# Kernel tuning notes

Hardware: AMD Instinct MI355X
Metric: run time of the kernel (lower is better)

## Reference

```python
import jax, jax.numpy as jnp
import numpy as np

B = 4096
LT = 30        # title_length
LE = 10        # max_entity_num
D = 300        # word/entity embedding dim
WORD_NUM = 100000
VERT_NUM = 18
H1, D1 = 20, 20   # Attention(20, 20) -> 400
H2, D2 = 5, 40    # Attention(5, 40)  -> 200
FUSE = H1 * D1 + H2 * D2   # 600
OUT = 400


def setup_inputs():
    key = jax.random.key(0)
    ks = jax.random.split(key, 24)
    s = 0.02
    inp = {
        'title_ids': jax.random.randint(ks[0], (B, LT), 0, WORD_NUM),
        'vert_ids': jax.random.randint(ks[1], (B,), 0, VERT_NUM + 1),
        'entity_ids': jax.random.randint(ks[2], (B, LE), 0, WORD_NUM),
        'word_table': jax.random.normal(ks[3], (WORD_NUM + 1, D), jnp.float32) * s,
        'vert_table': jax.random.normal(ks[4], (VERT_NUM + 1, 200), jnp.float32) * s,
        'entity_table': jax.random.normal(ks[5], (WORD_NUM, D), jnp.float32) * s,
        'WQ': jax.random.normal(ks[6], (D, H1 * D1), jnp.float32) * s,
        'WK': jax.random.normal(ks[7], (D, H1 * D1), jnp.float32) * s,
        'WV': jax.random.normal(ks[8], (D, H1 * D1), jnp.float32) * s,
        'WQ2': jax.random.normal(ks[9], (D, H2 * D2), jnp.float32) * s,
        'WK2': jax.random.normal(ks[10], (D, H2 * D2), jnp.float32) * s,
        'WV2': jax.random.normal(ks[11], (D, H2 * D2), jnp.float32) * s,
        'fc1_W': jax.random.normal(ks[12], (FUSE, OUT), jnp.float32) * s,
        'fc1_b': jnp.zeros((OUT,), jnp.float32),
        'fc2_W': jax.random.normal(ks[13], (FUSE, OUT), jnp.float32) * s,
        'fc2_b': jnp.zeros((OUT,), jnp.float32),
        'apt_W1': jax.random.normal(ks[14], (OUT, 200), jnp.float32) * s,
        'apt_b1': jnp.zeros((200,), jnp.float32),
        'apt_w2': jax.random.normal(ks[15], (200,), jnp.float32) * s,
        'ape_W1': jax.random.normal(ks[16], (OUT, 200), jnp.float32) * s,
        'ape_b1': jnp.zeros((200,), jnp.float32),
        'ape_w2': jax.random.normal(ks[17], (200,), jnp.float32) * s,
        'fc3_W': jax.random.normal(ks[18], (OUT + OUT + 200, OUT), jnp.float32) * s,
        'fc3_b': jnp.zeros((OUT,), jnp.float32),
    }
    return inp


def _mha(q_in, k_in, v_in, WQ, WK, WV, h, d):
    # q_in: [B,Lq,D]; k_in/v_in: [B,Lk,D] -> out [B,Lq,h*d]
    b, lq, _ = q_in.shape
    lk = k_in.shape[1]
    Q = (q_in @ WQ).reshape(b, lq, h, d)
    K = (k_in @ WK).reshape(b, lk, h, d)
    V = (v_in @ WV).reshape(b, lk, h, d)
    scores = jnp.einsum('bqhd,bkhd->bhqk', Q, K) / jnp.sqrt(jnp.asarray(d, Q.dtype))
    attn = jax.nn.softmax(scores, axis=-1)
    out = jnp.einsum('bhqk,bkhd->bqhd', attn, V)
    return out.reshape(b, lq, h * d)


def _att_pool(x, W1, b1, w2):
    # x: [B,L,F] -> [B,F]
    a = jax.nn.softmax(jnp.tanh(x @ W1 + b1) @ w2, axis=1)  # [B,L]
    return jnp.einsum('bl,blf->bf', a, x)


def reference(title_ids, vert_ids, entity_ids, word_table, vert_table, entity_table,
              WQ, WK, WV, WQ2, WK2, WV2, fc1_W, fc1_b, fc2_W, fc2_b,
              apt_W1, apt_b1, apt_w2, ape_W1, ape_b1, ape_w2, fc3_W, fc3_b):
    # Dropout is identity at inference.
    vert_vec = vert_table[vert_ids]              # [B,200]
    title_emb = word_table[title_ids]            # [B,LT,D]
    entity_emb = entity_table[entity_ids]        # [B,LE,D]

    # Cross (co-)attention, shared Attention2(5,40) weights
    title_co = _mha(title_emb, entity_emb, entity_emb, WQ2, WK2, WV2, H2, D2)   # [B,LT,200]
    entity_co = _mha(entity_emb, title_emb, title_emb, WQ2, WK2, WV2, H2, D2)   # [B,LE,200]

    # Self attention, shared Attention(20,20) weights
    title_vecs = _mha(title_emb, title_emb, title_emb, WQ, WK, WV, H1, D1)      # [B,LT,400]
    title_vecs = jnp.concatenate([title_vecs, title_co], axis=-1) @ fc1_W + fc1_b  # [B,LT,400]
    title_vec = _att_pool(title_vecs, apt_W1, apt_b1, apt_w2)                   # [B,400]

    entity_vecs = _mha(entity_emb, entity_emb, entity_emb, WQ, WK, WV, H1, D1)  # [B,LE,400]
    entity_vecs = jnp.concatenate([entity_vecs, entity_co], axis=-1) @ fc2_W + fc2_b
    entity_vec = _att_pool(entity_vecs, ape_W1, ape_b1, ape_w2)                 # [B,400]

    news_vec = jnp.concatenate([title_vec, entity_vec, vert_vec], axis=-1)      # [B,1000]
    return news_vec @ fc3_W + fc3_b                                             # [B,400]
```

## Files before the change

kernel.cpp:

```cpp
#include <hip/hip_runtime.h>
#include <hip/hip_bf16.h>

typedef unsigned short u16b;
typedef __attribute__((ext_vector_type(8))) short bf16x8;
typedef __attribute__((ext_vector_type(4))) float f32x4;

__device__ __forceinline__ float b2f(u16b u) { return __uint_as_float(((unsigned)u) << 16); }
__device__ __forceinline__ u16b f2b(float f) {
    unsigned u = __float_as_uint(f);
    unsigned r = u + 0x7fffu + ((u >> 16) & 1u);
    return (u16b)(r >> 16);
}
__device__ __forceinline__ int pk2(float a, float b) {
    return (int)f2b(a) | ((int)f2b(b) << 16);
}

__device__ __forceinline__ void async16(const u16b* g, u16b* l) {
    __builtin_amdgcn_global_load_lds(
        (const __attribute__((address_space(1))) unsigned int*)g,
        (__attribute__((address_space(3))) unsigned int*)l,
        16, 0, 0);
}

#define BATCH 4096
#define NPROJ 1920

__global__ void pack_wcatT(const float* __restrict__ WQ, const float* __restrict__ WK,
                           const float* __restrict__ WV, const float* __restrict__ WQ2,
                           const float* __restrict__ WK2, const float* __restrict__ WV2,
                           u16b* __restrict__ Wt) {
    int idx = blockIdx.x * 256 + threadIdx.x;
    if (idx >= 1920 * 320) return;
    int n = idx / 320, k = idx % 320;
    float v = 0.0f;
    if (k < 300 && n < 1800) {
        if      (n < 400)  v = WQ [k * 400 + n];
        else if (n < 800)  v = WK [k * 400 + (n - 400)];
        else if (n < 1200) v = WV [k * 400 + (n - 800)];
        else if (n < 1400) v = WQ2[k * 200 + (n - 1200)];
        else if (n < 1600) v = WK2[k * 200 + (n - 1400)];
        else               v = WV2[k * 200 + (n - 1600)];
    }
    Wt[idx] = f2b(v);
}

__global__ void pack_wt(const float* __restrict__ W, u16b* __restrict__ Wt,
                        int K, int N, int Kp, int Npad) {
    int idx = blockIdx.x * 256 + threadIdx.x;
    if (idx >= Npad * Kp) return;
    int n = idx / Kp, k = idx % Kp;
    Wt[idx] = f2b((k < K && n < N) ? W[k * N + n] : 0.0f);
}

__global__ void gather_bf16(const int* __restrict__ ids, const float* __restrict__ table,
                            u16b* __restrict__ Abuf, int nrows) {
    int idx = blockIdx.x * 256 + threadIdx.x;
    if (idx >= nrows * 40) return;
    int row = idx / 40, c = idx % 40;
    int k = c * 8;
    const float* src = table + (long long)ids[row] * 300;
    int4 v;
    if (k + 8 <= 300) {
        float4 f0 = *(const float4*)(src + k);
        float4 f1 = *(const float4*)(src + k + 4);
        v.x = pk2(f0.x, f0.y); v.y = pk2(f0.z, f0.w);
        v.z = pk2(f1.x, f1.y); v.w = pk2(f1.z, f1.w);
    } else if (k < 300) {
        float f[8];
        #pragma unroll
        for (int i = 0; i < 8; i++) f[i] = (k + i < 300) ? src[k + i] : 0.0f;
        v.x = pk2(f[0], f[1]); v.y = pk2(f[2], f[3]);
        v.z = pk2(f[4], f[5]); v.w = pk2(f[6], f[7]);
    } else {
        v.x = v.y = v.z = v.w = 0;
    }
    *(int4*)(Abuf + (long long)row * 320 + k) = v;
}

template<int HAS_BIAS, int DO_TANH>
__global__ __launch_bounds__(256) void gemm_mfma2(
        const u16b* __restrict__ A, long long lda,
        const u16b* __restrict__ Wt, int ldwt,
        const float* __restrict__ Bias,
        u16b* __restrict__ Out, long long ldo,
        int kiters, int N) {
    __shared__ __align__(16) u16b As[128 * 32];
    __shared__ __align__(16) u16b Bs[128 * 32];
    const int t = threadIdx.x, lane = t & 63, w = t >> 6;
    const int wm = w & 1, wn = w >> 1;
    const long long m0 = (long long)blockIdx.y * 128;
    const int n0 = blockIdx.x * 128;

    const int r0 = w * 32 + (lane >> 2);
    const int r1 = r0 + 16;
    const int cch = ((lane & 3) ^ ((r0 >> 1) & 3)) * 8;
    const u16b* gA0 = A + (m0 + r0) * lda + cch;
    const u16b* gA1 = A + (m0 + r1) * lda + cch;
    const u16b* gB0 = Wt + (long long)(n0 + r0) * ldwt + cch;
    const u16b* gB1 = Wt + (long long)(n0 + r1) * ldwt + cch;
    u16b* lA0 = &As[(w * 32) * 32];
    u16b* lA1 = &As[(w * 32 + 16) * 32];
    u16b* lB0 = &Bs[(w * 32) * 32];
    u16b* lB1 = &Bs[(w * 32 + 16) * 32];

    const int lr = lane & 15;
    const int kq8 = lane >> 4;
    const int slot = (kq8 ^ ((lr >> 1) & 3)) * 8;
    const u16b* aBase = &As[(wm * 64 + lr) * 32 + slot];
    const u16b* bBase = &Bs[(wn * 64 + lr) * 32 + slot];

    f32x4 acc[4][4];
    const f32x4 zf = {0.f, 0.f, 0.f, 0.f};
    #pragma unroll
    for (int mi = 0; mi < 4; mi++)
        #pragma unroll
        for (int ni = 0; ni < 4; ni++) acc[mi][ni] = zf;

    for (int it = 0; it < kiters; ++it) {
        async16(gA0, lA0); async16(gA1, lA1);
        async16(gB0, lB0); async16(gB1, lB1);
        gA0 += 32; gA1 += 32; gB0 += 32; gB1 += 32;
        __syncthreads();
        bf16x8 af[4], bf[4];
        #pragma unroll
        for (int mi = 0; mi < 4; mi++) af[mi] = *(const bf16x8*)(aBase + mi * 16 * 32);
        #pragma unroll
        for (int ni = 0; ni < 4; ni++) bf[ni] = *(const bf16x8*)(bBase + ni * 16 * 32);
        #pragma unroll
        for (int mi = 0; mi < 4; mi++)
            #pragma unroll
            for (int ni = 0; ni < 4; ni++)
                acc[mi][ni] = __builtin_amdgcn_mfma_f32_16x16x32_bf16(af[mi], bf[ni], acc[mi][ni], 0, 0, 0);
        __syncthreads();
    }

    const int cl = lane & 15;
    const int rb = (lane >> 4) * 4;
    #pragma unroll
    for (int ni = 0; ni < 4; ni++) {
        const int col = n0 + wn * 64 + ni * 16 + cl;
        if (col >= N) continue;
        const float bias = HAS_BIAS ? Bias[col] : 0.0f;
        #pragma unroll
        for (int mi = 0; mi < 4; mi++) {
            #pragma unroll
            for (int r = 0; r < 4; r++) {
                const long long row = m0 + wm * 64 + mi * 16 + rb + r;
                float v = acc[mi][ni][r] + bias;
                if (DO_TANH) v = tanhf(v);
                Out[row * ldo + col] = f2b(v);
            }
        }
    }
}

__global__ __launch_bounds__(256) void gemm_fc3(const float* __restrict__ tvec,
                                                const float* __restrict__ evec,
                                                const float* __restrict__ vtab,
                                                const int* __restrict__ vids,
                                                const float* __restrict__ W,
                                                const float* __restrict__ Bias,
                                                float* __restrict__ Out) {
    __shared__ float As[20][64];
    __shared__ float Bs[20][128];
    __shared__ int svid[64];
    const int t  = threadIdx.x;
    const int n0 = blockIdx.x * 128;
    const int m0 = blockIdx.y * 64;
    if (t < 64) svid[t] = vids[m0 + t];
    __syncthreads();
    const int r = t >> 2, k0 = (t & 3) * 5;
    const int bn = t & 127, bks = t >> 7;
    const int ty = t >> 4, tx = t & 15;
    float acc[4][8] = {};
    const int rr = m0 + r;
    for (int ks = 0; ks < 1000; ks += 20) {
        float av[5];
        #pragma unroll
        for (int i = 0; i < 5; i++) {
            int k = ks + k0 + i;
            float a;
            if (k < 400)      a = tvec[rr * 400 + k];
            else if (k < 800) a = evec[rr * 400 + (k - 400)];
            else              a = vtab[svid[r] * 200 + (k - 800)];
            av[i] = a;
        }
        float bv[10];
        const int nn = n0 + bn;
        #pragma unroll
        for (int i = 0; i < 10; i++)
            bv[i] = (nn < 400) ? W[(ks + i * 2 + bks) * 400 + nn] : 0.0f;
        __syncthreads();
        #pragma unroll
        for (int i = 0; i < 5; i++) As[k0 + i][r] = av[i];
        #pragma unroll
        for (int i = 0; i < 10; i++) Bs[i * 2 + bks][bn] = bv[i];
        __syncthreads();
        #pragma unroll
        for (int kk = 0; kk < 20; kk++) {
            const float4 a4  = *(const float4*)(&As[kk][ty * 4]);
            const float4 b4a = *(const float4*)(&Bs[kk][tx * 4]);
            const float4 b4b = *(const float4*)(&Bs[kk][tx * 4 + 64]);
            const float aa[4] = {a4.x, a4.y, a4.z, a4.w};
            const float bb[8] = {b4a.x, b4a.y, b4a.z, b4a.w, b4b.x, b4b.y, b4b.z, b4b.w};
            #pragma unroll
            for (int i = 0; i < 4; i++)
                #pragma unroll
                for (int j = 0; j < 8; j++) acc[i][j] = fmaf(aa[i], bb[j], acc[i][j]);
        }
    }
    #pragma unroll
    for (int i = 0; i < 4; i++) {
        long long orow = (long long)(m0 + ty * 4 + i) * 400;
        #pragma unroll
        for (int j = 0; j < 8; j++) {
            int nn = n0 + ((j < 4) ? (tx * 4 + j) : (64 + tx * 4 + j - 4));
            if (nn < 400) Out[orow + nn] = acc[i][j] + Bias[nn];
        }
    }
}

__global__ __launch_bounds__(256) void attn_title(const u16b* __restrict__ Tproj,
                                                  const u16b* __restrict__ Eproj,
                                                  u16b* __restrict__ Tcat) {
    __shared__ u16b sm[24000];
    const int b = blockIdx.x, t = threadIdx.x;
    for (int idx = t; idx < 12000; idx += 256) {
        int i = idx / 400, c = idx % 400;
        long long base = (long long)(b * 30 + i) * NPROJ;
        sm[idx]         = Tproj[base + 400 + c];
        sm[12000 + idx] = Tproj[base + 800 + c];
    }
    __syncthreads();
    const float scale1 = 0.22360679774997896f;
    for (int row = t; row < 600; row += 256) {
        int h = row / 30, i = row % 30;
        float q[20];
        const u16b* qrow = Tproj + (long long)(b * 30 + i) * NPROJ + h * 20;
        #pragma unroll
        for (int c = 0; c < 20; c++) q[c] = b2f(qrow[c]);
        float s[30];
        float mx = -1e30f;
        #pragma unroll
        for (int j = 0; j < 30; j++) {
            float a = 0.0f;
            #pragma unroll
            for (int c = 0; c < 20; c++) a += q[c] * b2f(sm[j * 400 + h * 20 + c]);
            s[j] = a * scale1;
            mx = fmaxf(mx, s[j]);
        }
        float sum = 0.0f;
        #pragma unroll
        for (int j = 0; j < 30; j++) { s[j] = __expf(s[j] - mx); sum += s[j]; }
        float inv = 1.0f / sum;
        #pragma unroll
        for (int c = 0; c < 20; c++) {
            float o = 0.0f;
            #pragma unroll
            for (int j = 0; j < 30; j++) o += s[j] * b2f(sm[12000 + j * 400 + h * 20 + c]);
            Tcat[(long long)(b * 30 + i) * 608 + h * 20 + c] = f2b(o * inv);
        }
    }
    __syncthreads();
    for (int idx = t; idx < 2000; idx += 256) {
        int j = idx / 200, c = idx % 200;
        long long base = (long long)(b * 10 + j) * NPROJ;
        sm[idx]        = Eproj[base + 1400 + c];
        sm[2000 + idx] = Eproj[base + 1600 + c];
    }
    __syncthreads();
    const float scale2 = 0.15811388300841897f;
    if (t < 150) {
        int h = t / 30, i = t % 30;
        float q[40];
        const u16b* qrow = Tproj + (long long)(b * 30 + i) * NPROJ + 1200 + h * 40;
        #pragma unroll
        for (int c = 0; c < 40; c++) q[c] = b2f(qrow[c]);
        float s[10];
        float mx = -1e30f;
        #pragma unroll
        for (int j = 0; j < 10; j++) {
            float a = 0.0f;
            #pragma unroll
            for (int c = 0; c < 40; c++) a += q[c] * b2f(sm[j * 200 + h * 40 + c]);
            s[j] = a * scale2;
            mx = fmaxf(mx, s[j]);
        }
        float sum = 0.0f;
        #pragma unroll
        for (int j = 0; j < 10; j++) { s[j] = __expf(s[j] - mx); sum += s[j]; }
        float inv = 1.0f / sum;
        #pragma unroll
        for (int c = 0; c < 40; c++) {
            float o = 0.0f;
            #pragma unroll
            for (int j = 0; j < 10; j++) o += s[j] * b2f(sm[2000 + j * 200 + h * 40 + c]);
            Tcat[(long long)(b * 30 + i) * 608 + 400 + h * 40 + c] = f2b(o * inv);
        }
    }
}

__global__ __launch_bounds__(256) void attn_entity(const u16b* __restrict__ Tproj,
                                                   const u16b* __restrict__ Eproj,
                                                   u16b* __restrict__ Ecat) {
    __shared__ u16b sm[12000];
    const int b = blockIdx.x, t = threadIdx.x;
    for (int idx = t; idx < 4000; idx += 256) {
        int i = idx / 400, c = idx % 400;
        long long base = (long long)(b * 10 + i) * NPROJ;
        sm[idx]        = Eproj[base + 400 + c];
        sm[4000 + idx] = Eproj[base + 800 + c];
    }
    __syncthreads();
    const float scale1 = 0.22360679774997896f;
    if (t < 200) {
        int h = t / 10, i = t % 10;
        float q[20];
        const u16b* qrow = Eproj + (long long)(b * 10 + i) * NPROJ + h * 20;
        #pragma unroll
        for (int c = 0; c < 20; c++) q[c] = b2f(qrow[c]);
        float s[10];
        float mx = -1e30f;
        #pragma unroll
        for (int j = 0; j < 10; j++) {
            float a = 0.0f;
            #pragma unroll
            for (int c = 0; c < 20; c++) a += q[c] * b2f(sm[j * 400 + h * 20 + c]);
            s[j] = a * scale1;
            mx = fmaxf(mx, s[j]);
        }
        float sum = 0.0f;
        #pragma unroll
        for (int j = 0; j < 10; j++) { s[j] = __expf(s[j] - mx); sum += s[j]; }
        float inv = 1.0f / sum;
        #pragma unroll
        for (int c = 0; c < 20; c++) {
            float o = 0.0f;
            #pragma unroll
            for (int j = 0; j < 10; j++) o += s[j] * b2f(sm[4000 + j * 400 + h * 20 + c]);
            Ecat[(long long)(b * 10 + i) * 608 + h * 20 + c] = f2b(o * inv);
        }
    }
    __syncthreads();
    for (int idx = t; idx < 6000; idx += 256) {
        int j = idx / 200, c = idx % 200;
        long long base = (long long)(b * 30 + j) * NPROJ;
        sm[idx]        = Tproj[base + 1400 + c];
        sm[6000 + idx] = Tproj[base + 1600 + c];
    }
    __syncthreads();
    const float scale2 = 0.15811388300841897f;
    if (t < 50) {
        int h = t / 10, i = t % 10;
        float q[40];
        const u16b* qrow = Eproj + (long long)(b * 10 + i) * NPROJ + 1200 + h * 40;
        #pragma unroll
        for (int c = 0; c < 40; c++) q[c] = b2f(qrow[c]);
        float s[30];
        float mx = -1e30f;
        #pragma unroll
        for (int j = 0; j < 30; j++) {
            float a = 0.0f;
            #pragma unroll
            for (int c = 0; c < 40; c++) a += q[c] * b2f(sm[j * 200 + h * 40 + c]);
            s[j] = a * scale2;
            mx = fmaxf(mx, s[j]);
        }
        float sum = 0.0f;
        #pragma unroll
        for (int j = 0; j < 30; j++) { s[j] = __expf(s[j] - mx); sum += s[j]; }
        float inv = 1.0f / sum;
        #pragma unroll
        for (int c = 0; c < 40; c++) {
            float o = 0.0f;
            #pragma unroll
            for (int j = 0; j < 30; j++) o += s[j] * b2f(sm[6000 + j * 200 + h * 40 + c]);
            Ecat[(long long)(b * 10 + i) * 608 + 400 + h * 40 + c] = f2b(o * inv);
        }
    }
}

template <int L>
__global__ __launch_bounds__(256) void pool_finalize(const u16b* __restrict__ P,
                                                     const u16b* __restrict__ Vv,
                                                     const float* __restrict__ w2,
                                                     float* __restrict__ outv) {
    __shared__ float sred[L][8];
    __shared__ float sa[L];
    const int b = blockIdx.x, t = threadIdx.x;
    const int i = t / 8, u = t % 8;
    if (i < L) {
        float p = 0.0f;
        const u16b* Pr = P + (long long)(b * L + i) * 200 + u * 25;
        const float* wr = w2 + u * 25;
        #pragma unroll
        for (int c = 0; c < 25; c++) p += b2f(Pr[c]) * wr[c];
        sred[i][u] = p;
    }
    __syncthreads();
    if (t == 0) {
        float s[L];
        float mx = -1e30f;
        for (int ii = 0; ii < L; ii++) {
            float v = 0.0f;
            for (int uu = 0; uu < 8; uu++) v += sred[ii][uu];
            s[ii] = v;
            mx = fmaxf(mx, v);
        }
        float sum = 0.0f;
        for (int ii = 0; ii < L; ii++) { s[ii] = __expf(s[ii] - mx); sum += s[ii]; }
        float inv = 1.0f / sum;
        for (int ii = 0; ii < L; ii++) sa[ii] = s[ii] * inv;
    }
    __syncthreads();
    for (int f = t; f < 400; f += 256) {
        float o = 0.0f;
        #pragma unroll
        for (int ii = 0; ii < L; ii++) o += sa[ii] * b2f(Vv[(long long)(b * L + ii) * 400 + f]);
        outv[(long long)b * 400 + f] = o;
    }
}

extern "C" void kernel_launch(void* const* d_in, const int* in_sizes, int n_in,
                              void* d_out, int out_size, void* d_ws, size_t ws_size,
                              hipStream_t stream) {
    const int*   title_ids  = (const int*)d_in[0];
    const int*   vert_ids   = (const int*)d_in[1];
    const int*   entity_ids = (const int*)d_in[2];
    const float* word_table = (const float*)d_in[3];
    const float* vert_table = (const float*)d_in[4];
    const float* entity_table = (const float*)d_in[5];
    const float* WQ  = (const float*)d_in[6];
    const float* WK  = (const float*)d_in[7];
    const float* WV  = (const float*)d_in[8];
    const float* WQ2 = (const float*)d_in[9];
    const float* WK2 = (const float*)d_in[10];
    const float* WV2 = (const float*)d_in[11];
    const float* fc1_W = (const float*)d_in[12];
    const float* fc1_b = (const float*)d_in[13];
    const float* fc2_W = (const float*)d_in[14];
    const float* fc2_b = (const float*)d_in[15];
    const float* apt_W1 = (const float*)d_in[16];
    const float* apt_b1 = (const float*)d_in[17];
    const float* apt_w2 = (const float*)d_in[18];
    const float* ape_W1 = (const float*)d_in[19];
    const float* ape_b1 = (const float*)d_in[20];
    const float* ape_w2 = (const float*)d_in[21];
    const float* fc3_W = (const float*)d_in[22];
    const float* fc3_b = (const float*)d_in[23];

    const long long OFF_WCATT = 0;
    const long long OFF_FC1WT = 1228800ll;
    const long long OFF_FC2WT = OFF_FC1WT + 622592ll;
    const long long OFF_APTWT = OFF_FC2WT + 622592ll;
    const long long OFF_APEWT = OFF_APTWT + 212992ll;
    const long long OFF_TVEC  = OFF_APEWT + 212992ll;
    const long long OFF_EVEC  = OFF_TVEC + 6553600ll;
    const long long fixedB    = OFF_EVEC + 6553600ll;

    int C = BATCH;
    while (C > 64 && fixedB + (long long)C * 227840ll > (long long)ws_size) C >>= 1;

    char* ws = (char*)d_ws;
    const long long OFF_ABUFT = fixedB;
    const long long OFF_ABUFE = OFF_ABUFT + (long long)C * 19200ll;
    const long long OFF_TPROJ = OFF_ABUFE + (long long)C * 6400ll;
    const long long OFF_EPROJ = OFF_TPROJ + (long long)C * 115200ll;
    const long long OFF_TCAT  = OFF_EPROJ + (long long)C * 38400ll;
    const long long OFF_ECAT  = OFF_TCAT  + (long long)C * 36480ll;
    const long long OFF_TV = OFF_ABUFT;
    const long long OFF_EV = OFF_ABUFT + (long long)C * 24000ll;
    const long long OFF_PT = OFF_EPROJ;
    const long long OFF_PE = OFF_EPROJ + (long long)C * 12000ll;

    u16b*  wcatT = (u16b*)(ws + OFF_WCATT);
    u16b*  fc1Wt = (u16b*)(ws + OFF_FC1WT);
    u16b*  fc2Wt = (u16b*)(ws + OFF_FC2WT);
    u16b*  aptWt = (u16b*)(ws + OFF_APTWT);
    u16b*  apeWt = (u16b*)(ws + OFF_APEWT);
    float* tvec  = (float*)(ws + OFF_TVEC);
    float* evec  = (float*)(ws + OFF_EVEC);
    u16b*  AbufT = (u16b*)(ws + OFF_ABUFT);
    u16b*  AbufE = (u16b*)(ws + OFF_ABUFE);
    u16b*  Tproj = (u16b*)(ws + OFF_TPROJ);
    u16b*  Eproj = (u16b*)(ws + OFF_EPROJ);
    u16b*  Tcat  = (u16b*)(ws + OFF_TCAT);
    u16b*  Ecat  = (u16b*)(ws + OFF_ECAT);
    u16b*  Tv    = (u16b*)(ws + OFF_TV);
    u16b*  Ev    = (u16b*)(ws + OFF_EV);
    u16b*  Pt    = (u16b*)(ws + OFF_PT);
    u16b*  Pe    = (u16b*)(ws + OFF_PE);
    float* outp  = (float*)d_out;

    pack_wcatT<<<(1920 * 320 + 255) / 256, 256, 0, stream>>>(WQ, WK, WV, WQ2, WK2, WV2, wcatT);
    pack_wt<<<(512 * 608 + 255) / 256, 256, 0, stream>>>(fc1_W, fc1Wt, 600, 400, 608, 512);
    pack_wt<<<(512 * 608 + 255) / 256, 256, 0, stream>>>(fc2_W, fc2Wt, 600, 400, 608, 512);
    pack_wt<<<(256 * 416 + 255) / 256, 256, 0, stream>>>(apt_W1, aptWt, 400, 200, 416, 256);
    pack_wt<<<(256 * 416 + 255) / 256, 256, 0, stream>>>(ape_W1, apeWt, 400, 200, 416, 256);

    for (int c0 = 0; c0 < BATCH; c0 += C) {
        const int MT = C * 30, ME = C * 10;
        gather_bf16<<<(MT * 40 + 255) / 256, 256, 0, stream>>>(
            title_ids + (long long)c0 * 30, word_table, AbufT, MT);
        gather_bf16<<<(ME * 40 + 255) / 256, 256, 0, stream>>>(
            entity_ids + (long long)c0 * 10, entity_table, AbufE, ME);
        gemm_mfma2<0, 0><<<dim3(15, MT / 128), 256, 0, stream>>>(
            AbufT, 320, wcatT, 320, nullptr, Tproj, NPROJ, 10, 1800);
        gemm_mfma2<0, 0><<<dim3(15, ME / 128), 256, 0, stream>>>(
            AbufE, 320, wcatT, 320, nullptr, Eproj, NPROJ, 10, 1800);
        attn_title<<<C, 256, 0, stream>>>(Tproj, Eproj, Tcat);
        attn_entity<<<C, 256, 0, stream>>>(Tproj, Eproj, Ecat);
        gemm_mfma2<1, 0><<<dim3(4, MT / 128), 256, 0, stream>>>(
            Tcat, 608, fc1Wt, 608, fc1_b, Tv, 400, 19, 400);
        gemm_mfma2<1, 0><<<dim3(4, ME / 128), 256, 0, stream>>>(
            Ecat, 608, fc2Wt, 608, fc2_b, Ev, 400, 19, 400);
        gemm_mfma2<1, 1><<<dim3(2, MT / 128), 256, 0, stream>>>(
            Tv, 400, aptWt, 416, apt_b1, Pt, 200, 13, 200);
        gemm_mfma2<1, 1><<<dim3(2, ME / 128), 256, 0, stream>>>(
            Ev, 400, apeWt, 416, ape_b1, Pe, 200, 13, 200);
        pool_finalize<30><<<C, 256, 0, stream>>>(Pt, Tv, apt_w2, tvec + (long long)c0 * 400);
        pool_finalize<10><<<C, 256, 0, stream>>>(Pe, Ev, ape_w2, evec + (long long)c0 * 400);
    }
    gemm_fc3<<<dim3(4, BATCH / 64), 256, 0, stream>>>(tvec, evec, vert_table, vert_ids, fc3_W, fc3_b, outp);
}
```

Baseline: 2.180 ms.

## Move fc3 onto MFMA GEMM with bf16 concat buffer; vectorize attention loads

Replaces the scalar fp32 fc3 GEMM with the bf16 MFMA GEMM (now templated for fp32 output). The pooled title/entity vectors and vertical embeddings are written straight into a padded bf16 concat buffer. Separately, the attention kernels now stage K/V into shared memory with 16-byte loads and unpack bf16 pairs from wide shared loads instead of scalar reads. It also restructures the PV accumulation as a per-key outer-product loop. This adds a bf16 rounding of the fc3 input and weights.

```diff
diff --git a/kernel.cpp b/kernel.cpp
--- a/kernel.cpp
+++ b/kernel.cpp
@@ -13,6 +13,10 @@
 }
 __device__ __forceinline__ int pk2(float a, float b) {
     return (int)f2b(a) | ((int)f2b(b) << 16);
+}
+__device__ __forceinline__ void up2(int p, float& a, float& b) {
+    a = __uint_as_float(((unsigned)p) << 16);
+    b = __uint_as_float(((unsigned)p) & 0xffff0000u);
 }
 
 __device__ __forceinline__ void async16(const u16b* g, u16b* l) {
@@ -52,6 +56,16 @@
     Wt[idx] = f2b((k < K && n < N) ? W[k * N + n] : 0.0f);
 }
 
+__global__ void pack_vert(const int* __restrict__ vids, const float* __restrict__ vtab,
+                          u16b* __restrict__ Acat) {
+    int idx = blockIdx.x * 256 + threadIdx.x;
+    if (idx >= BATCH * 224) return;
+    int b = idx / 224, c = idx % 224;
+    u16b v = 0;
+    if (c < 200) v = f2b(vtab[(long long)vids[b] * 200 + c]);
+    Acat[(long long)b * 1024 + 800 + c] = v;
+}
+
 __global__ void gather_bf16(const int* __restrict__ ids, const float* __restrict__ table,
                             u16b* __restrict__ Abuf, int nrows) {
     int idx = blockIdx.x * 256 + threadIdx.x;
@@ -77,12 +91,12 @@
     *(int4*)(Abuf + (long long)row * 320 + k) = v;
 }
 
-template<int HAS_BIAS, int DO_TANH>
+template<int HAS_BIAS, int DO_TANH, int F32OUT>
 __global__ __launch_bounds__(256) void gemm_mfma2(
         const u16b* __restrict__ A, long long lda,
         const u16b* __restrict__ Wt, int ldwt,
         const float* __restrict__ Bias,
-        u16b* __restrict__ Out, long long ldo,
+        void* __restrict__ OutV, long long ldo,
         int kiters, int N) {
     __shared__ __align__(16) u16b As[128 * 32];
     __shared__ __align__(16) u16b Bs[128 * 32];
@@ -148,74 +162,9 @@
                 const long long row = m0 + wm * 64 + mi * 16 + rb + r;
                 float v = acc[mi][ni][r] + bias;
                 if (DO_TANH) v = tanhf(v);
-                Out[row * ldo + col] = f2b(v);
-            }
-        }
-    }
-}
-
-__global__ __launch_bounds__(256) void gemm_fc3(const float* __restrict__ tvec,
-                                                const float* __restrict__ evec,
-                                                const float* __restrict__ vtab,
-                                                const int* __restrict__ vids,
-                                                const float* __restrict__ W,
-                                                const float* __restrict__ Bias,
-                                                float* __restrict__ Out) {
-    __shared__ float As[20][64];
-    __shared__ float Bs[20][128];
-    __shared__ int svid[64];
-    const int t  = threadIdx.x;
-    const int n0 = blockIdx.x * 128;
-    const int m0 = blockIdx.y * 64;
-    if (t < 64) svid[t] = vids[m0 + t];
-    __syncthreads();
-    const int r = t >> 2, k0 = (t & 3) * 5;
-    const int bn = t & 127, bks = t >> 7;
-    const int ty = t >> 4, tx = t & 15;
-    float acc[4][8] = {};
-    const int rr = m0 + r;
-    for (int ks = 0; ks < 1000; ks += 20) {
-        float av[5];
-        #pragma unroll
-        for (int i = 0; i < 5; i++) {
-            int k = ks + k0 + i;
-            float a;
-            if (k < 400)      a = tvec[rr * 400 + k];
-            else if (k < 800) a = evec[rr * 400 + (k - 400)];
-            else              a = vtab[svid[r] * 200 + (k - 800)];
-            av[i] = a;
-        }
-        float bv[10];
-        const int nn = n0 + bn;
-        #pragma unroll
-        for (int i = 0; i < 10; i++)
-            bv[i] = (nn < 400) ? W[(ks + i * 2 + bks) * 400 + nn] : 0.0f;
-        __syncthreads();
-        #pragma unroll
-        for (int i = 0; i < 5; i++) As[k0 + i][r] = av[i];
-        #pragma unroll
-        for (int i = 0; i < 10; i++) Bs[i * 2 + bks][bn] = bv[i];
-        __syncthreads();
-        #pragma unroll
-        for (int kk = 0; kk < 20; kk++) {
-            const float4 a4  = *(const float4*)(&As[kk][ty * 4]);
-            const float4 b4a = *(const float4*)(&Bs[kk][tx * 4]);
-            const float4 b4b = *(const float4*)(&Bs[kk][tx * 4 + 64]);
-            const float aa[4] = {a4.x, a4.y, a4.z, a4.w};
-            const float bb[8] = {b4a.x, b4a.y, b4a.z, b4a.w, b4b.x, b4b.y, b4b.z, b4b.w};
-            #pragma unroll
-            for (int i = 0; i < 4; i++)
-                #pragma unroll
-                for (int j = 0; j < 8; j++) acc[i][j] = fmaf(aa[i], bb[j], acc[i][j]);
-        }
-    }
-    #pragma unroll
-    for (int i = 0; i < 4; i++) {
-        long long orow = (long long)(m0 + ty * 4 + i) * 400;
-        #pragma unroll
-        for (int j = 0; j < 8; j++) {
-            int nn = n0 + ((j < 4) ? (tx * 4 + j) : (64 + tx * 4 + j - 4));
-            if (nn < 400) Out[orow + nn] = acc[i][j] + Bias[nn];
+                if (F32OUT) ((float*)OutV)[row * ldo + col] = v;
+                else        ((u16b*)OutV)[row * ldo + col] = f2b(v);
+            }
         }
     }
 }
@@ -223,160 +172,244 @@
 __global__ __launch_bounds__(256) void attn_title(const u16b* __restrict__ Tproj,
                                                   const u16b* __restrict__ Eproj,
                                                   u16b* __restrict__ Tcat) {
-    __shared__ u16b sm[24000];
+    __shared__ __align__(16) u16b sm[24000];
     const int b = blockIdx.x, t = threadIdx.x;
-    for (int idx = t; idx < 12000; idx += 256) {
-        int i = idx / 400, c = idx % 400;
-        long long base = (long long)(b * 30 + i) * NPROJ;
-        sm[idx]         = Tproj[base + 400 + c];
-        sm[12000 + idx] = Tproj[base + 800 + c];
+    const u16b* baseT = Tproj + (long long)b * 30 * NPROJ;
+    for (int c = t; c < 3000; c += 256) {
+        int half = c / 1500, cc = c % 1500;
+        int row = cc / 50, off = (cc % 50) * 8;
+        int4 v = *(const int4*)(baseT + (long long)row * NPROJ + (half ? 800 : 400) + off);
+        *(int4*)(&sm[half * 12000 + row * 400 + off]) = v;
     }
     __syncthreads();
     const float scale1 = 0.22360679774997896f;
-    for (int row = t; row < 600; row += 256) {
-        int h = row / 30, i = row % 30;
+    for (int rh = t; rh < 600; rh += 256) {
+        int h = rh / 30, i = rh % 30;
+        const u16b* qp = baseT + (long long)i * NPROJ + h * 20;
         float q[20];
-        const u16b* qrow = Tproj + (long long)(b * 30 + i) * NPROJ + h * 20;
-        #pragma unroll
-        for (int c = 0; c < 20; c++) q[c] = b2f(qrow[c]);
-        float s[30];
-        float mx = -1e30f;
+        #pragma unroll
+        for (int u = 0; u < 5; u++) {
+            int2 pp = *(const int2*)(qp + u * 4);
+            up2(pp.x, q[u*4+0], q[u*4+1]); up2(pp.y, q[u*4+2], q[u*4+3]);
+        }
+        float s[30]; float mx = -1e30f;
         #pragma unroll
         for (int j = 0; j < 30; j++) {
+            const u16b* kp = &sm[j * 400 + h * 20];
             float a = 0.0f;
             #pragma unroll
-            for (int c = 0; c < 20; c++) a += q[c] * b2f(sm[j * 400 + h * 20 + c]);
-            s[j] = a * scale1;
-            mx = fmaxf(mx, s[j]);
+            for (int u = 0; u < 5; u++) {
+                int2 pp = *(const int2*)(kp + u * 4);
+                float x0,x1,x2,x3; up2(pp.x,x0,x1); up2(pp.y,x2,x3);
+                a += q[u*4]*x0 + q[u*4+1]*x1 + q[u*4+2]*x2 + q[u*4+3]*x3;
+            }
+            s[j] = a * scale1; mx = fmaxf(mx, s[j]);
         }
         float sum = 0.0f;
         #pragma unroll
         for (int j = 0; j < 30; j++) { s[j] = __expf(s[j] - mx); sum += s[j]; }
         float inv = 1.0f / sum;
         #pragma unroll
-        for (int c = 0; c < 20; c++) {
-            float o = 0.0f;
-            #pragma unroll
-            for (int j = 0; j < 30; j++) o += s[j] * b2f(sm[12000 + j * 400 + h * 20 + c]);
-            Tcat[(long long)(b * 30 + i) * 608 + h * 20 + c] = f2b(o * inv);
-        }
-    }
-    __syncthreads();
-    for (int idx = t; idx < 2000; idx += 256) {
-        int j = idx / 200, c = idx % 200;
-        long long base = (long long)(b * 10 + j) * NPROJ;
-        sm[idx]        = Eproj[base + 1400 + c];
-        sm[2000 + idx] = Eproj[base + 1600 + c];
+        for (int j = 0; j < 30; j++) s[j] *= inv;
+        float o[20] = {};
+        #pragma unroll
+        for (int j = 0; j < 30; j++) {
+            const u16b* vp = &sm[12000 + j * 400 + h * 20];
+            float sj = s[j];
+            #pragma unroll
+            for (int u = 0; u < 5; u++) {
+                int2 pp = *(const int2*)(vp + u * 4);
+                float x0,x1,x2,x3; up2(pp.x,x0,x1); up2(pp.y,x2,x3);
+                o[u*4]   = fmaf(sj, x0, o[u*4]);
+                o[u*4+1] = fmaf(sj, x1, o[u*4+1]);
+                o[u*4+2] = fmaf(sj, x2, o[u*4+2]);
+                o[u*4+3] = fmaf(sj, x3, o[u*4+3]);
+            }
+        }
+        u16b* op = Tcat + (long long)(b * 30 + i) * 608 + h * 20;
+        #pragma unroll
+        for (int u = 0; u < 10; u++) *(int*)(op + u * 2) = pk2(o[u*2], o[u*2+1]);
+    }
+    __syncthreads();
+    const u16b* baseE = Eproj + (long long)b * 10 * NPROJ;
+    for (int c = t; c < 500; c += 256) {
+        int half = c / 250, cc = c % 250;
+        int row = cc / 25, off = (cc % 25) * 8;
+        int4 v = *(const int4*)(baseE + (long long)row * NPROJ + (half ? 1600 : 1400) + off);
+        *(int4*)(&sm[half * 2000 + row * 200 + off]) = v;
     }
     __syncthreads();
     const float scale2 = 0.15811388300841897f;
     if (t < 150) {
         int h = t / 30, i = t % 30;
+        const u16b* qp = baseT + (long long)i * NPROJ + 1200 + h * 40;
         float q[40];
-        const u16b* qrow = Tproj + (long long)(b * 30 + i) * NPROJ + 1200 + h * 40;
-        #pragma unroll
-        for (int c = 0; c < 40; c++) q[c] = b2f(qrow[c]);
-        float s[10];
-        float mx = -1e30f;
+        #pragma unroll
+        for (int u = 0; u < 10; u++) {
+            int2 pp = *(const int2*)(qp + u * 4);
+            up2(pp.x, q[u*4+0], q[u*4+1]); up2(pp.y, q[u*4+2], q[u*4+3]);
+        }
+        float s[10]; float mx = -1e30f;
         #pragma unroll
         for (int j = 0; j < 10; j++) {
+            const u16b* kp = &sm[j * 200 + h * 40];
             float a = 0.0f;
             #pragma unroll
-            for (int c = 0; c < 40; c++) a += q[c] * b2f(sm[j * 200 + h * 40 + c]);
-            s[j] = a * scale2;
-            mx = fmaxf(mx, s[j]);
+            for (int u = 0; u < 5; u++) {
+                int4 pp = *(const int4*)(kp + u * 8);
+                float x0,x1,x2,x3,x4,x5,x6,x7;
+                up2(pp.x,x0,x1); up2(pp.y,x2,x3); up2(pp.z,x4,x5); up2(pp.w,x6,x7);
+                a += q[u*8]*x0 + q[u*8+1]*x1 + q[u*8+2]*x2 + q[u*8+3]*x3
+                   + q[u*8+4]*x4 + q[u*8+5]*x5 + q[u*8+6]*x6 + q[u*8+7]*x7;
+            }
+            s[j] = a * scale2; mx = fmaxf(mx, s[j]);
         }
         float sum = 0.0f;
         #pragma unroll
         for (int j = 0; j < 10; j++) { s[j] = __expf(s[j] - mx); sum += s[j]; }
         float inv = 1.0f / sum;
         #pragma unroll
-        for (int c = 0; c < 40; c++) {
-            float o = 0.0f;
-            #pragma unroll
-            for (int j = 0; j < 10; j++) o += s[j] * b2f(sm[2000 + j * 200 + h * 40 + c]);
-            Tcat[(long long)(b * 30 + i) * 608 + 400 + h * 40 + c] = f2b(o * inv);
-        }
+        for (int j = 0; j < 10; j++) s[j] *= inv;
+        float o[40] = {};
+        #pragma unroll
+        for (int j = 0; j < 10; j++) {
+            const u16b* vp = &sm[2000 + j * 200 + h * 40];
+            float sj = s[j];
+            #pragma unroll
+            for (int u = 0; u < 5; u++) {
+                int4 pp = *(const int4*)(vp + u * 8);
+                float x0,x1,x2,x3,x4,x5,x6,x7;
+                up2(pp.x,x0,x1); up2(pp.y,x2,x3); up2(pp.z,x4,x5); up2(pp.w,x6,x7);
+                o[u*8]   = fmaf(sj, x0, o[u*8]);   o[u*8+1] = fmaf(sj, x1, o[u*8+1]);
+                o[u*8+2] = fmaf(sj, x2, o[u*8+2]); o[u*8+3] = fmaf(sj, x3, o[u*8+3]);
+                o[u*8+4] = fmaf(sj, x4, o[u*8+4]); o[u*8+5] = fmaf(sj, x5, o[u*8+5]);
+                o[u*8+6] = fmaf(sj, x6, o[u*8+6]); o[u*8+7] = fmaf(sj, x7, o[u*8+7]);
+            }
+        }
+        u16b* op = Tcat + (long long)(b * 30 + i) * 608 + 400 + h * 40;
+        #pragma unroll
+        for (int u = 0; u < 20; u++) *(int*)(op + u * 2) = pk2(o[u*2], o[u*2+1]);
     }
 }
 
 __global__ __launch_bounds__(256) void attn_entity(const u16b* __restrict__ Tproj,
                                                    const u16b* __restrict__ Eproj,
                                                    u16b* __restrict__ Ecat) {
-    __shared__ u16b sm[12000];
+    __shared__ __align__(16) u16b sm[12000];
     const int b = blockIdx.x, t = threadIdx.x;
-    for (int idx = t; idx < 4000; idx += 256) {
-        int i = idx / 400, c = idx % 400;
-        long long base = (long long)(b * 10 + i) * NPROJ;
-        sm[idx]        = Eproj[base + 400 + c];
-        sm[4000 + idx] = Eproj[base + 800 + c];
+    const u16b* baseE = Eproj + (long long)b * 10 * NPROJ;
+    const u16b* baseT = Tproj + (long long)b * 30 * NPROJ;
+    for (int c = t; c < 1000; c += 256) {
+        int half = c / 500, cc = c % 500;
+        int row = cc / 50, off = (cc % 50) * 8;
+        int4 v = *(const int4*)(baseE + (long long)row * NPROJ + (half ? 800 : 400) + off);
+        *(int4*)(&sm[half * 4000 + row * 400 + off]) = v;
     }
     __syncthreads();
     const float scale1 = 0.22360679774997896f;
     if (t < 200) {
         int h = t / 10, i = t % 10;
+        const u16b* qp = baseE + (long long)i * NPROJ + h * 20;
         float q[20];
-        const u16b* qrow = Eproj + (long long)(b * 10 + i) * NPROJ + h * 20;
-        #pragma unroll
-        for (int c = 0; c < 20; c++) q[c] = b2f(qrow[c]);
-        float s[10];
-        float mx = -1e30f;
+        #pragma unroll
+        for (int u = 0; u < 5; u++) {
+            int2 pp = *(const int2*)(qp + u * 4);
+            up2(pp.x, q[u*4+0], q[u*4+1]); up2(pp.y, q[u*4+2], q[u*4+3]);
+        }
+        float s[10]; float mx = -1e30f;
         #pragma unroll
         for (int j = 0; j < 10; j++) {
+            const u16b* kp = &sm[j * 400 + h * 20];
             float a = 0.0f;
             #pragma unroll
-            for (int c = 0; c < 20; c++) a += q[c] * b2f(sm[j * 400 + h * 20 + c]);
-            s[j] = a * scale1;
-            mx = fmaxf(mx, s[j]);
+            for (int u = 0; u < 5; u++) {
+                int2 pp = *(const int2*)(kp + u * 4);
+                float x0,x1,x2,x3; up2(pp.x,x0,x1); up2(pp.y,x2,x3);
+                a += q[u*4]*x0 + q[u*4+1]*x1 + q[u*4+2]*x2 + q[u*4+3]*x3;
+            }
+            s[j] = a * scale1; mx = fmaxf(mx, s[j]);
         }
         float sum = 0.0f;
         #pragma unroll
         for (int j = 0; j < 10; j++) { s[j] = __expf(s[j] - mx); sum += s[j]; }
         float inv = 1.0f / sum;
         #pragma unroll
-        for (int c = 0; c < 20; c++) {
-            float o = 0.0f;
-            #pragma unroll
-            for (int j = 0; j < 10; j++) o += s[j] * b2f(sm[4000 + j * 400 + h * 20 + c]);
-            Ecat[(long long)(b * 10 + i) * 608 + h * 20 + c] = f2b(o * inv);
-        }
-    }
-    __syncthreads();
-    for (int idx = t; idx < 6000; idx += 256) {
-        int j = idx / 200, c = idx % 200;
-        long long base = (long long)(b * 30 + j) * NPROJ;
-        sm[idx]        = Tproj[base + 1400 + c];
-        sm[6000 + idx] = Tproj[base + 1600 + c];
+        for (int j = 0; j < 10; j++) s[j] *= inv;
+        float o[20] = {};
+        #pragma unroll
+        for (int j = 0; j < 10; j++) {
+            const u16b* vp = &sm[4000 + j * 400 + h * 20];
+            float sj = s[j];
+            #pragma unroll
+            for (int u = 0; u < 5; u++) {
+                int2 pp = *(const int2*)(vp + u * 4);
+                float x0,x1,x2,x3; up2(pp.x,x0,x1); up2(pp.y,x2,x3);
+                o[u*4]   = fmaf(sj, x0, o[u*4]);   o[u*4+1] = fmaf(sj, x1, o[u*4+1]);
+                o[u*4+2] = fmaf(sj, x2, o[u*4+2]); o[u*4+3] = fmaf(sj, x3, o[u*4+3]);
+            }
+        }
+        u16b* op = Ecat + (long long)(b * 10 + i) * 608 + h * 20;
+        #pragma unroll
+        for (int u = 0; u < 10; u++) *(int*)(op + u * 2) = pk2(o[u*2], o[u*2+1]);
+    }
+    __syncthreads();
+    for (int c = t; c < 1500; c += 256) {
+        int half = c / 750, cc = c % 750;
+        int row = cc / 25, off = (cc % 25) * 8;
+        int4 v = *(const int4*)(baseT + (long long)row * NPROJ + (half ? 1600 : 1400) + off);
+        *(int4*)(&sm[half * 6000 + row * 200 + off]) = v;
     }
     __syncthreads();
     const float scale2 = 0.15811388300841897f;
     if (t < 50) {
         int h = t / 10, i = t % 10;
+        const u16b* qp = baseE + (long long)i * NPROJ + 1200 + h * 40;
         float q[40];
-        const u16b* qrow = Eproj + (long long)(b * 10 + i) * NPROJ + 1200 + h * 40;
-        #pragma unroll
-        for (int c = 0; c < 40; c++) q[c] = b2f(qrow[c]);
-        float s[30];
-        float mx = -1e30f;
+        #pragma unroll
+        for (int u = 0; u < 10; u++) {
+            int2 pp = *(const int2*)(qp + u * 4);
+            up2(pp.x, q[u*4+0], q[u*4+1]); up2(pp.y, q[u*4+2], q[u*4+3]);
+        }
+        float s[30]; float mx = -1e30f;
         #pragma unroll
         for (int j = 0; j < 30; j++) {
+            const u16b* kp = &sm[j * 200 + h * 40];
             float a = 0.0f;
             #pragma unroll
-            for (int c = 0; c < 40; c++) a += q[c] * b2f(sm[j * 200 + h * 40 + c]);
-            s[j] = a * scale2;
-            mx = fmaxf(mx, s[j]);
+            for (int u = 0; u < 5; u++) {
+                int4 pp = *(const int4*)(kp + u * 8);
+                float x0,x1,x2,x3,x4,x5,x6,x7;
+                up2(pp.x,x0,x1); up2(pp.y,x2,x3); up2(pp.z,x4,x5); up2(pp.w,x6,x7);
+                a += q[u*8]*x0 + q[u*8+1]*x1 + q[u*8+2]*x2 + q[u*8+3]*x3
+                   + q[u*8+4]*x4 + q[u*8+5]*x5 + q[u*8+6]*x6 + q[u*8+7]*x7;
+            }
+            s[j] = a * scale2; mx = fmaxf(mx, s[j]);
         }
         float sum = 0.0f;
         #pragma unroll
         for (int j = 0; j < 30; j++) { s[j] = __expf(s[j] - mx); sum += s[j]; }
         float inv = 1.0f / sum;
         #pragma unroll
-        for (int c = 0; c < 40; c++) {
-            float o = 0.0f;
-            #pragma unroll
-            for (int j = 0; j < 30; j++) o += s[j] * b2f(sm[6000 + j * 200 + h * 40 + c]);
-            Ecat[(long long)(b * 10 + i) * 608 + 400 + h * 40 + c] = f2b(o * inv);
-        }
+        for (int j = 0; j < 30; j++) s[j] *= inv;
+        float o[40] = {};
+        #pragma unroll
+        for (int j = 0; j < 30; j++) {
+            const u16b* vp = &sm[6000 + j * 200 + h * 40];
+            float sj = s[j];
+            #pragma unroll
+            for (int u = 0; u < 5; u++) {
+                int4 pp = *(const int4*)(vp + u * 8);
+                float x0,x1,x2,x3,x4,x5,x6,x7;
+                up2(pp.x,x0,x1); up2(pp.y,x2,x3); up2(pp.z,x4,x5); up2(pp.w,x6,x7);
+                o[u*8]   = fmaf(sj, x0, o[u*8]);   o[u*8+1] = fmaf(sj, x1, o[u*8+1]);
+                o[u*8+2] = fmaf(sj, x2, o[u*8+2]); o[u*8+3] = fmaf(sj, x3, o[u*8+3]);
+                o[u*8+4] = fmaf(sj, x4, o[u*8+4]); o[u*8+5] = fmaf(sj, x5, o[u*8+5]);
+                o[u*8+6] = fmaf(sj, x6, o[u*8+6]); o[u*8+7] = fmaf(sj, x7, o[u*8+7]);
+            }
+        }
+        u16b* op = Ecat + (long long)(b * 10 + i) * 608 + 400 + h * 40;
+        #pragma unroll
+        for (int u = 0; u < 20; u++) *(int*)(op + u * 2) = pk2(o[u*2], o[u*2+1]);
     }
 }
 
@@ -384,7 +417,7 @@
 __global__ __launch_bounds__(256) void pool_finalize(const u16b* __restrict__ P,
                                                      const u16b* __restrict__ Vv,
                                                      const float* __restrict__ w2,
-                                                     float* __restrict__ outv) {
+                                                     u16b* __restrict__ outv) {
     __shared__ float sred[L][8];
     __shared__ float sa[L];
     const int b = blockIdx.x, t = threadIdx.x;
@@ -417,7 +450,7 @@
         float o = 0.0f;
         #pragma unroll
         for (int ii = 0; ii < L; ii++) o += sa[ii] * b2f(Vv[(long long)(b * L + ii) * 400 + f]);
-        outv[(long long)b * 400 + f] = o;
+        outv[(long long)b * 1024 + f] = f2b(o);
     }
 }
 
@@ -454,9 +487,9 @@
     const long long OFF_FC2WT = OFF_FC1WT + 622592ll;
     const long long OFF_APTWT = OFF_FC2WT + 622592ll;
     const long long OFF_APEWT = OFF_APTWT + 212992ll;
-    const long long OFF_TVEC  = OFF_APEWT + 212992ll;
-    const long long OFF_EVEC  = OFF_TVEC + 6553600ll;
-    const long long fixedB    = OFF_EVEC + 6553600ll;
+    const long long OFF_FC3WT = OFF_APEWT + 212992ll;
+    const long long OFF_ACAT  = OFF_FC3WT + 1048576ll;
+    const long long fixedB    = OFF_ACAT + 8388608ll;
 
     int C = BATCH;
     while (C > 64 && fixedB + (long long)C * 227840ll > (long long)ws_size) C >>= 1;
@@ -478,8 +511,8 @@
     u16b*  fc2Wt = (u16b*)(ws + OFF_FC2WT);
     u16b*  aptWt = (u16b*)(ws + OFF_APTWT);
     u16b*  apeWt = (u16b*)(ws + OFF_APEWT);
-    float* tvec  = (float*)(ws + OFF_TVEC);
-    float* evec  = (float*)(ws + OFF_EVEC);
+    u16b*  fc3Wt = (u16b*)(ws + OFF_FC3WT);
+    u16b*  Acat  = (u16b*)(ws + OFF_ACAT);
     u16b*  AbufT = (u16b*)(ws + OFF_ABUFT);
     u16b*  AbufE = (u16b*)(ws + OFF_ABUFE);
     u16b*  Tproj = (u16b*)(ws + OFF_TPROJ);
@@ -490,13 +523,14 @@
     u16b*  Ev    = (u16b*)(ws + OFF_EV);
     u16b*  Pt    = (u16b*)(ws + OFF_PT);
     u16b*  Pe    = (u16b*)(ws + OFF_PE);
-    float* outp  = (float*)d_out;
 
     pack_wcatT<<<(1920 * 320 + 255) / 256, 256, 0, stream>>>(WQ, WK, WV, WQ2, WK2, WV2, wcatT);
     pack_wt<<<(512 * 608 + 255) / 256, 256, 0, stream>>>(fc1_W, fc1Wt, 600, 400, 608, 512);
     pack_wt<<<(512 * 608 + 255) / 256, 256, 0, stream>>>(fc2_W, fc2Wt, 600, 400, 608, 512);
     pack_wt<<<(256 * 416 + 255) / 256, 256, 0, stream>>>(apt_W1, aptWt, 400, 200, 416, 256);
     pack_wt<<<(256 * 416 + 255) / 256, 256, 0, stream>>>(ape_W1, apeWt, 400, 200, 416, 256);
+    pack_wt<<<(512 * 1024 + 255) / 256, 256, 0, stream>>>(fc3_W, fc3Wt, 1000, 400, 1024, 512);
+    pack_vert<<<(BATCH * 224 + 255) / 256, 256, 0, stream>>>(vert_ids, vert_table, Acat);
 
     for (int c0 = 0; c0 < BATCH; c0 += C) {
         const int MT = C * 30, ME = C * 10;
@@ -504,22 +538,23 @@
             title_ids + (long long)c0 * 30, word_table, AbufT, MT);
         gather_bf16<<<(ME * 40 + 255) / 256, 256, 0, stream>>>(
             entity_ids + (long long)c0 * 10, entity_table, AbufE, ME);
-        gemm_mfma2<0, 0><<<dim3(15, MT / 128), 256, 0, stream>>>(
+        gemm_mfma2<0, 0, 0><<<dim3(15, MT / 128), 256, 0, stream>>>(
             AbufT, 320, wcatT, 320, nullptr, Tproj, NPROJ, 10, 1800);
-        gemm_mfma2<0, 0><<<dim3(15, ME / 128), 256, 0, stream>>>(
+        gemm_mfma2<0, 0, 0><<<dim3(15, ME / 128), 256, 0, stream>>>(
             AbufE, 320, wcatT, 320, nullptr, Eproj, NPROJ, 10, 1800);
         attn_title<<<C, 256, 0, stream>>>(Tproj, Eproj, Tcat);
         attn_entity<<<C, 256, 0, stream>>>(Tproj, Eproj, Ecat);
-        gemm_mfma2<1, 0><<<dim3(4, MT / 128), 256, 0, stream>>>(
+        gemm_mfma2<1, 0, 0><<<dim3(4, MT / 128), 256, 0, stream>>>(
             Tcat, 608, fc1Wt, 608, fc1_b, Tv, 400, 19, 400);
-        gemm_mfma2<1, 0><<<dim3(4, ME / 128), 256, 0, stream>>>(
+        gemm_mfma2<1, 0, 0><<<dim3(4, ME / 128), 256, 0, stream>>>(
             Ecat, 608, fc2Wt, 608, fc2_b, Ev, 400, 19, 400);
-        gemm_mfma2<1, 1><<<dim3(2, MT / 128), 256, 0, stream>>>(
+        gemm_mfma2<1, 1, 0><<<dim3(2, MT / 128), 256, 0, stream>>>(
             Tv, 400, aptWt, 416, apt_b1, Pt, 200, 13, 200);
-        gemm_mfma2<1, 1><<<dim3(2, ME / 128), 256, 0, stream>>>(
+        gemm_mfma2<1, 1, 0><<<dim3(2, ME / 128), 256, 0, stream>>>(
             Ev, 400, apeWt, 416, ape_b1, Pe, 200, 13, 200);
-        pool_finalize<30><<<C, 256, 0, stream>>>(Pt, Tv, apt_w2, tvec + (long long)c0 * 400);
-        pool_finalize<10><<<C, 256, 0, stream>>>(Pe, Ev, ape_w2, evec + (long long)c0 * 400);
-    }
-    gemm_fc3<<<dim3(4, BATCH / 64), 256, 0, stream>>>(tvec, evec, vert_table, vert_ids, fc3_W, fc3_b, outp);
-}
+        pool_finalize<30><<<C, 256, 0, stream>>>(Pt, Tv, apt_w2, Acat + (long long)c0 * 1024);
+        pool_finalize<10><<<C, 256, 0, stream>>>(Pe, Ev, ape_w2, Acat + (long long)c0 * 1024 + 400);
+    }
+    gemm_mfma2<1, 0, 1><<<dim3(4, BATCH / 128), 256, 0, stream>>>(
+        Acat, 1024, fc3Wt, 1024, fc3_b, d_out, 400, 32, 400);
+}
```

Measured after the change: 2.587 ms. 1.19x slower.
